# Kernel tuning notes

Measured on AMD Instinct MI355X. Metric: run time of the kernel, lower is better.

Reference implementation:

```python
import jax, jax.numpy as jnp
import numpy as np

C1 = 0.01 ** 2
C2 = 0.03 ** 2
EPS = 1e-8


def _box3(t):
    # 3x3 mean filter, zero padding (SAME), NCHW, 1 channel.
    k = jnp.full((1, 1, 3, 3), 1.0 / 9.0, dtype=t.dtype)
    return jax.lax.conv_general_dilated(
        t, k, window_strides=(1, 1), padding=((1, 1), (1, 1)),
        dimension_numbers=("NCHW", "OIHW", "NCHW"))


def setup_inputs() -> dict:
    key = jax.random.key(0)
    k1, k2 = jax.random.split(key)
    shape = (32, 1, 1024, 1024)
    x = jax.random.uniform(k1, shape, dtype=jnp.float32)
    y = jax.random.uniform(k2, shape, dtype=jnp.float32)
    return {"x": x, "y": y}


def reference(x, y):
    mu_x = _box3(x)
    mu_y = _box3(y)
    sigma_x = _box3(x * x) - mu_x * mu_x
    sigma_y = _box3(y * y) - mu_y * mu_y
    sigma_xy = _box3(x * y) - mu_x * mu_y
    ssim_map = ((2.0 * mu_x * mu_y + C1) * (2.0 * sigma_xy + C2)
                / ((mu_x ** 2 + mu_y ** 2 + C1) * (sigma_x + sigma_y + C2) + EPS))
    return 1.0 - jnp.mean(ssim_map)
```

## Files before the change

kernel.cpp:

```cpp
#include <hip/hip_runtime.h>

#define IMG_H 1024
#define IMG_W 1024
#define RPB   8
#define TPB   256

struct HS { float x[4], y[4], xx[4], yy[4], xy[4]; };

__device__ __forceinline__ void zero_hs(HS& h)
{
#pragma unroll
    for (int j = 0; j < 4; ++j) { h.x[j]=0.f; h.y[j]=0.f; h.xx[j]=0.f; h.yy[j]=0.f; h.xy[j]=0.f; }
}

__device__ __forceinline__ void hsum6(float xl, float4 xv, float xr6,
                                      float yl, float4 yv, float yr6, HS& h)
{
    float xs[6] = { xl, xv.x, xv.y, xv.z, xv.w, xr6 };
    float ys[6] = { yl, yv.x, yv.y, yv.z, yv.w, yr6 };

    float pxx[6], pyy[6], pxy[6];
#pragma unroll
    for (int k = 0; k < 6; ++k) {
        pxx[k] = xs[k] * xs[k];
        pyy[k] = ys[k] * ys[k];
        pxy[k] = xs[k] * ys[k];
    }
#pragma unroll
    for (int j = 0; j < 4; ++j) {
        h.x[j]  = xs[j]  + xs[j + 1]  + xs[j + 2];
        h.y[j]  = ys[j]  + ys[j + 1]  + ys[j + 2];
        h.xx[j] = pxx[j] + pxx[j + 1] + pxx[j + 2];
        h.yy[j] = pyy[j] + pyy[j + 1] + pyy[j + 2];
        h.xy[j] = pxy[j] + pxy[j + 1] + pxy[j + 2];
    }
}

__device__ __forceinline__ void accum(const HS& A, const HS& B, const HS& C, float& acc)
{
    const float c1s  = 81.0f * 1e-4f;
    const float c2s  = 81.0f * 9e-4f;
    const float epss = 6561.0f * 1e-8f;
#pragma unroll
    for (int j = 0; j < 4; ++j) {
        const float sx  = A.x[j]  + B.x[j]  + C.x[j];
        const float sy  = A.y[j]  + B.y[j]  + C.y[j];
        const float sxx = A.xx[j] + B.xx[j] + C.xx[j];
        const float syy = A.yy[j] + B.yy[j] + C.yy[j];
        const float sxy = A.xy[j] + B.xy[j] + C.xy[j];

        const float t1 = sx * sy;
        const float t2 = fmaf(sx, sx, sy * sy);
        const float s2 = sxx + syy;
        const float An = fmaf(2.0f, t1, c1s);
        const float Bn = fmaf(-2.0f, t1, fmaf(18.0f, sxy, c2s));
        const float Xd = t2 + c1s;
        const float Yd = fmaf(9.0f, s2, c2s - t2);
        const float den = fmaf(Xd, Yd, epss);
        const float num = An * Bn;
        acc = fmaf(num, __builtin_amdgcn_rcpf(den), acc);
    }
}

__global__ __launch_bounds__(TPB, 4)
void ssim_map_sum_kernel(const float* __restrict__ x,
                         const float* __restrict__ y,
                         float* __restrict__ part)
{
    const int rb = blockIdx.x;
    const int n  = blockIdx.y;
    const int r0 = rb * RPB;
    const int c  = (int)threadIdx.x * 4;

    const int   cl = (c > 0) ? c - 1 : 0;
    const int   cr = (c + 4 < IMG_W) ? c + 4 : IMG_W - 1;
    const float lm = (c > 0) ? 1.0f : 0.0f;
    const float rm = (c + 4 < IMG_W) ? 1.0f : 0.0f;

    const float* xi = x + (size_t)n * IMG_H * IMG_W;
    const float* yi = y + (size_t)n * IMG_H * IMG_W;

    HS hA, hB, hC;

    if (r0 > 0) {
        const float* xr = xi + (size_t)(r0 - 1) * IMG_W;
        const float* yr = yi + (size_t)(r0 - 1) * IMG_W;
        hsum6(xr[cl] * lm, *reinterpret_cast<const float4*>(xr + c), xr[cr] * rm,
              yr[cl] * lm, *reinterpret_cast<const float4*>(yr + c), yr[cr] * rm, hA);
    } else {
        zero_hs(hA);
    }
    {
        const float* xr = xi + (size_t)r0 * IMG_W;
        const float* yr = yi + (size_t)r0 * IMG_W;
        hsum6(xr[cl] * lm, *reinterpret_cast<const float4*>(xr + c), xr[cr] * rm,
              yr[cl] * lm, *reinterpret_cast<const float4*>(yr + c), yr[cr] * rm, hB);
    }

    float4 pxa, pya, pxb, pyb;
    float  xla, xra, yla, yra, xlb, xrb, ylb, yrb;
    {
        const float* xr = xi + (size_t)(r0 + 1) * IMG_W;
        const float* yr = yi + (size_t)(r0 + 1) * IMG_W;
        pxa = *reinterpret_cast<const float4*>(xr + c);
        pya = *reinterpret_cast<const float4*>(yr + c);
        xla = xr[cl]; xra = xr[cr];
        yla = yr[cl]; yra = yr[cr];
    }

    float acc = 0.0f;

#define STEP_MAIN(k, PXI, PYI, XLI, XRI, YLI, YRI, PXO, PYO, XLO, XRO, YLO, YRO, P, Q, R) \
    {                                                                              \
        const float* xw = xi + (size_t)(r0 + (k) + 2) * IMG_W;                     \
        const float* yw = yi + (size_t)(r0 + (k) + 2) * IMG_W;                     \
        PXO = *reinterpret_cast<const float4*>(xw + c);                            \
        PYO = *reinterpret_cast<const float4*>(yw + c);                            \
        XLO = xw[cl]; XRO = xw[cr];                                                \
        YLO = yw[cl]; YRO = yw[cr];                                                \
        hsum6(XLI * lm, PXI, XRI * rm, YLI * lm, PYI, YRI * rm, R);                \
        accum(P, Q, R, acc);                                                       \
    }

    STEP_MAIN(0, pxa, pya, xla, xra, yla, yra, pxb, pyb, xlb, xrb, ylb, yrb, hA, hB, hC)
    STEP_MAIN(1, pxb, pyb, xlb, xrb, ylb, yrb, pxa, pya, xla, xra, yla, yra, hB, hC, hA)
    STEP_MAIN(2, pxa, pya, xla, xra, yla, yra, pxb, pyb, xlb, xrb, ylb, yrb, hC, hA, hB)
    STEP_MAIN(3, pxb, pyb, xlb, xrb, ylb, yrb, pxa, pya, xla, xra, yla, yra, hA, hB, hC)
    STEP_MAIN(4, pxa, pya, xla, xra, yla, yra, pxb, pyb, xlb, xrb, ylb, yrb, hB, hC, hA)
    STEP_MAIN(5, pxb, pyb, xlb, xrb, ylb, yrb, pxa, pya, xla, xra, yla, yra, hC, hA, hB)
#undef STEP_MAIN

    {
        const int rr = (r0 + 8 < IMG_H) ? r0 + 8 : IMG_H - 1;
        const float* xw = xi + (size_t)rr * IMG_W;
        const float* yw = yi + (size_t)rr * IMG_W;
        pxb = *reinterpret_cast<const float4*>(xw + c);
        pyb = *reinterpret_cast<const float4*>(yw + c);
        xlb = xw[cl]; xrb = xw[cr];
        ylb = yw[cl]; yrb = yw[cr];
        hsum6(xla * lm, pxa, xra * rm, yla * lm, pya, yra * rm, hC);
        accum(hA, hB, hC, acc);
    }

    {
        const float rwm = (r0 + 8 < IMG_H) ? 1.0f : 0.0f;
        float4 xv = pxb, yv = pyb;
        xv.x *= rwm; xv.y *= rwm; xv.z *= rwm; xv.w *= rwm;
        yv.x *= rwm; yv.y *= rwm; yv.z *= rwm; yv.w *= rwm;
        hsum6(xlb * (lm * rwm), xv, xrb * (rm * rwm),
              ylb * (lm * rwm), yv, yrb * (rm * rwm), hA);
        accum(hB, hC, hA, acc);
    }

#pragma unroll
    for (int off = 32; off > 0; off >>= 1)
        acc += __shfl_down(acc, off);

    __shared__ float red[TPB / 64];
    const int lane = (int)threadIdx.x & 63;
    const int wave = (int)threadIdx.x >> 6;
    if (lane == 0) red[wave] = acc;
    __syncthreads();
    if (threadIdx.x == 0) {
        float s = 0.0f;
#pragma unroll
        for (int w = 0; w < TPB / 64; ++w) s += red[w];
        part[blockIdx.y * gridDim.x + blockIdx.x] = s;
    }
}

__global__ __launch_bounds__(256)
void ssim_finalize_kernel(const float* __restrict__ part, int nparts,
                          float* __restrict__ out, float inv_count)
{
    float s = 0.0f;
    for (int i = (int)threadIdx.x; i < nparts; i += 256)
        s += part[i];
#pragma unroll
    for (int off = 32; off > 0; off >>= 1)
        s += __shfl_down(s, off);

    __shared__ float red[4];
    const int lane = (int)threadIdx.x & 63;
    const int wave = (int)threadIdx.x >> 6;
    if (lane == 0) red[wave] = s;
    __syncthreads();
    if (threadIdx.x == 0) {
        float t = red[0] + red[1] + red[2] + red[3];
        out[0] = 1.0f - t * inv_count;
    }
}

extern "C" void kernel_launch(void* const* d_in, const int* in_sizes, int n_in,
                              void* d_out, int out_size, void* d_ws, size_t ws_size,
                              hipStream_t stream)
{
    const float* x = (const float*)d_in[0];
    const float* y = (const float*)d_in[1];
    float* out  = (float*)d_out;
    float* part = (float*)d_ws;

    const long long total = (long long)in_sizes[0];
    const int N = (int)(total / ((long long)IMG_H * IMG_W));
    const int nparts = (IMG_H / RPB) * N;

    dim3 grid(IMG_H / RPB, N);
    ssim_map_sum_kernel<<<grid, TPB, 0, stream>>>(x, y, part);

    ssim_finalize_kernel<<<1, 256, 0, stream>>>(part, nparts, out, 1.0f / (float)total);
}
```

Before: 278.4 us.

## Double rows per block, remap workgroups across XCDs, raise occupancy bound

```diff
diff --git a/kernel.cpp b/kernel.cpp
--- a/kernel.cpp
+++ b/kernel.cpp
@@ -2,8 +2,9 @@
 
 #define IMG_H 1024
 #define IMG_W 1024
-#define RPB   8
+#define RPB   16
 #define TPB   256
+#define NBLK  ((IMG_H / RPB) * 32)
 
 struct HS { float x[4], y[4], xx[4], yy[4], xy[4]; };
 
@@ -62,13 +63,15 @@
     }
 }
 
-__global__ __launch_bounds__(TPB, 4)
+__global__ __launch_bounds__(TPB, 8)
 void ssim_map_sum_kernel(const float* __restrict__ x,
                          const float* __restrict__ y,
                          float* __restrict__ part)
 {
-    const int rb = blockIdx.x;
-    const int n  = blockIdx.y;
+    const int orig = (int)blockIdx.x;
+    const int wgid = (orig & 7) * (NBLK / 8) + (orig >> 3);
+    const int rb = wgid % (IMG_H / RPB);
+    const int n  = wgid / (IMG_H / RPB);
     const int r0 = rb * RPB;
     const int c  = (int)threadIdx.x * 4;
 
@@ -121,35 +124,47 @@
         hsum6(XLI * lm, PXI, XRI * rm, YLI * lm, PYI, YRI * rm, R);                \
         accum(P, Q, R, acc);                                                       \
     }
-
-    STEP_MAIN(0, pxa, pya, xla, xra, yla, yra, pxb, pyb, xlb, xrb, ylb, yrb, hA, hB, hC)
-    STEP_MAIN(1, pxb, pyb, xlb, xrb, ylb, yrb, pxa, pya, xla, xra, yla, yra, hB, hC, hA)
-    STEP_MAIN(2, pxa, pya, xla, xra, yla, yra, pxb, pyb, xlb, xrb, ylb, yrb, hC, hA, hB)
-    STEP_MAIN(3, pxb, pyb, xlb, xrb, ylb, yrb, pxa, pya, xla, xra, yla, yra, hA, hB, hC)
-    STEP_MAIN(4, pxa, pya, xla, xra, yla, yra, pxb, pyb, xlb, xrb, ylb, yrb, hB, hC, hA)
-    STEP_MAIN(5, pxb, pyb, xlb, xrb, ylb, yrb, pxa, pya, xla, xra, yla, yra, hC, hA, hB)
+#define STEP_A2B(k, P, Q, R) STEP_MAIN(k, pxa, pya, xla, xra, yla, yra, pxb, pyb, xlb, xrb, ylb, yrb, P, Q, R)
+#define STEP_B2A(k, P, Q, R) STEP_MAIN(k, pxb, pyb, xlb, xrb, ylb, yrb, pxa, pya, xla, xra, yla, yra, P, Q, R)
+
+    STEP_A2B(0,  hA, hB, hC)
+    STEP_B2A(1,  hB, hC, hA)
+    STEP_A2B(2,  hC, hA, hB)
+    STEP_B2A(3,  hA, hB, hC)
+    STEP_A2B(4,  hB, hC, hA)
+    STEP_B2A(5,  hC, hA, hB)
+    STEP_A2B(6,  hA, hB, hC)
+    STEP_B2A(7,  hB, hC, hA)
+    STEP_A2B(8,  hC, hA, hB)
+    STEP_B2A(9,  hA, hB, hC)
+    STEP_A2B(10, hB, hC, hA)
+    STEP_B2A(11, hC, hA, hB)
+    STEP_A2B(12, hA, hB, hC)
+    STEP_B2A(13, hB, hC, hA)
+#undef STEP_A2B
+#undef STEP_B2A
 #undef STEP_MAIN
 
     {
-        const int rr = (r0 + 8 < IMG_H) ? r0 + 8 : IMG_H - 1;
+        const int rr = (r0 + RPB < IMG_H) ? r0 + RPB : IMG_H - 1;
         const float* xw = xi + (size_t)rr * IMG_W;
         const float* yw = yi + (size_t)rr * IMG_W;
         pxb = *reinterpret_cast<const float4*>(xw + c);
         pyb = *reinterpret_cast<const float4*>(yw + c);
         xlb = xw[cl]; xrb = xw[cr];
         ylb = yw[cl]; yrb = yw[cr];
-        hsum6(xla * lm, pxa, xra * rm, yla * lm, pya, yra * rm, hC);
-        accum(hA, hB, hC, acc);
-    }
-
-    {
-        const float rwm = (r0 + 8 < IMG_H) ? 1.0f : 0.0f;
+        hsum6(xla * lm, pxa, xra * rm, yla * lm, pya, yra * rm, hB);
+        accum(hC, hA, hB, acc);
+    }
+
+    {
+        const float rwm = (r0 + RPB < IMG_H) ? 1.0f : 0.0f;
         float4 xv = pxb, yv = pyb;
         xv.x *= rwm; xv.y *= rwm; xv.z *= rwm; xv.w *= rwm;
         yv.x *= rwm; yv.y *= rwm; yv.z *= rwm; yv.w *= rwm;
         hsum6(xlb * (lm * rwm), xv, xrb * (rm * rwm),
-              ylb * (lm * rwm), yv, yrb * (rm * rwm), hA);
-        accum(hB, hC, hA, acc);
+              ylb * (lm * rwm), yv, yrb * (rm * rwm), hC);
+        accum(hA, hB, hC, acc);
     }
 
 #pragma unroll
@@ -165,7 +180,7 @@
         float s = 0.0f;
 #pragma unroll
         for (int w = 0; w < TPB / 64; ++w) s += red[w];
-        part[blockIdx.y * gridDim.x + blockIdx.x] = s;
+        part[blockIdx.x] = s;
     }
 }
 
@@ -204,8 +219,7 @@
     const int N = (int)(total / ((long long)IMG_H * IMG_W));
     const int nparts = (IMG_H / RPB) * N;
 
-    dim3 grid(IMG_H / RPB, N);
-    ssim_map_sum_kernel<<<grid, TPB, 0, stream>>>(x, y, part);
+    ssim_map_sum_kernel<<<dim3(nparts), TPB, 0, stream>>>(x, y, part);
 
     ssim_finalize_kernel<<<1, 256, 0, stream>>>(part, nparts, out, 1.0f / (float)total);
 }
```

Result: slower. 495.5 us (+78.0%).
